# Optimization experiments

Hardware: AMD Instinct MI355X
Metric: run time of the kernel (lower is better)

## Reference

```python
import jax, jax.numpy as jnp
import numpy as np

B, T, E, A = 4, 4096, 512, 64

def setup_inputs() -> dict:
    key = jax.random.key(0)
    k1, k2, k3, k4 = jax.random.split(key, 4)
    embedded = jax.random.normal(k1, (B, T, E), dtype=jnp.float32)
    # torch Linear(E, A, bias=False): weight [A, E], y = x @ W.T. Store as [E, A].
    s = 1.0 / np.sqrt(E)
    Wq = jax.random.uniform(k2, (E, A), dtype=jnp.float32, minval=-s, maxval=s)
    Wk = jax.random.uniform(k3, (E, A), dtype=jnp.float32, minval=-s, maxval=s)
    Wv = jax.random.uniform(k4, (E, A), dtype=jnp.float32, minval=-s, maxval=s)
    return {"embedded": embedded, "Wq": Wq, "Wk": Wk, "Wv": Wv}

def reference(embedded, Wq, Wk, Wv):
    Q = embedded @ Wq  # [B, T, A]
    K = embedded @ Wk
    V = embedded @ Wv
    A_dim = V.shape[-1]
    scores = jnp.einsum('btd,bsd->bts', Q, K) / jnp.sqrt(jnp.float32(A_dim))  # [B, T, T]
    Tlen = scores.shape[-1]
    causal = jnp.tril(jnp.ones((Tlen, Tlen), dtype=bool))
    scores = jnp.where(causal, scores, -jnp.inf)
    attn = jax.nn.softmax(scores, axis=-1)
    out = jnp.einsum('bts,bsd->btd', attn, V)  # [B, T, A]
    return jnp.round(out, 4)
```

## Files before the change

kernel.cpp:

```cpp
#include <hip/hip_runtime.h>

#define B_ 4
#define T_ 4096
#define E_ 512
#define A_ 64
#define SQSCALE 0.1803368801111204f

typedef __attribute__((ext_vector_type(8)))  short bf16x8;
typedef __attribute__((ext_vector_type(8)))  unsigned short ushort8;
typedef __attribute__((ext_vector_type(4)))  unsigned int   u32x4;
typedef __attribute__((ext_vector_type(4)))  float f32x4;
typedef __attribute__((ext_vector_type(16))) float f32x16;

__device__ __forceinline__ unsigned short f2bf(float x) {
    union { float f; unsigned int u; } v; v.f = x;
    unsigned int r = v.u + 0x7fffu + ((v.u >> 16) & 1u);
    return (unsigned short)(r >> 16);
}
__device__ __forceinline__ unsigned cvtpk(float a, float b) {
    unsigned r;
    asm("v_cvt_pk_bf16_f32 %0, %1, %2" : "=v"(r) : "v"(a), "v"(b));
    return r;
}
__device__ __forceinline__ void pls(unsigned &a, unsigned &b) {
    asm("v_permlane32_swap_b32 %0, %1" : "+v"(a), "+v"(b));
}

__global__ __launch_bounds__(256) void prep_w(
    const float* __restrict__ Wq, const float* __restrict__ Wk,
    const float* __restrict__ Wv, unsigned short* __restrict__ Wp)
{
    const int e = blockIdx.x * 256 + threadIdx.x;
    const int nt = e >> 10;
    const int ks = (e >> 6) & 15;
    const int l  = e & 63;
    const int col = nt * 16 + (l & 15);
    const int kb  = ks * 32 + (l >> 4) * 8;
    const float* W = (col < 64) ? Wq : ((col < 128) ? Wk : Wv);
    const int cc = col & 63;
    const float sc = (col < 64) ? SQSCALE : 1.f;
    union { unsigned short s[8]; ushort8 v; } u;
    #pragma unroll
    for (int j = 0; j < 8; ++j) u.s[j] = f2bf(W[(kb + j) * 64 + cc] * sc);
    *(ushort8*)&Wp[(size_t)e * 8] = u.v;
}

__global__ __launch_bounds__(512, 4) void qkv_proj_kernel(
    const float* __restrict__ emb, const unsigned short* __restrict__ Wp,
    unsigned short* __restrict__ Qo, unsigned short* __restrict__ Kp,
    unsigned short* __restrict__ Vp)
{
    __shared__ unsigned short at[32][536];
    __shared__ unsigned short kt[32][72];
    __shared__ unsigned short vt[64][40];
    const int tid = threadIdx.x;
    const long row0 = (long)blockIdx.x * 32;

    {
        const int r = tid >> 4, c16 = tid & 15;
        const float* __restrict__ src = emb + (row0 + r) * 512;
        #pragma unroll
        for (int j = 0; j < 4; ++j) {
            const int col = j * 128 + c16 * 8;
            const float4 x0 = *(const float4*)(src + col);
            const float4 x1 = *(const float4*)(src + col + 4);
            u32x4 p;
            p[0] = cvtpk(x0.x, x0.y); p[1] = cvtpk(x0.z, x0.w);
            p[2] = cvtpk(x1.x, x1.y); p[3] = cvtpk(x1.z, x1.w);
            *(u32x4*)&at[r][col] = p;
        }
    }
    __syncthreads();

    const int w = tid >> 6, lane = tid & 63;
    const int c = lane & 15, hi = lane >> 4;
    const int rg = w & 1, ng = w >> 1;

    f32x4 acc[3];
    #pragma unroll
    for (int j = 0; j < 3; ++j) acc[j] = (f32x4){0.f, 0.f, 0.f, 0.f};

    #pragma unroll
    for (int ks = 0; ks < 16; ++ks) {
        const bf16x8 af = *(const bf16x8*)&at[rg * 16 + c][ks * 32 + hi * 8];
        #pragma unroll
        for (int j = 0; j < 3; ++j) {
            const int nt = ng * 3 + j;
            const bf16x8 bf_ = *(const bf16x8*)&Wp[((size_t)(nt * 16 + ks) * 64 + lane) * 8];
            acc[j] = __builtin_amdgcn_mfma_f32_16x16x32_bf16(af, bf_, acc[j], 0, 0, 0);
        }
    }

    #pragma unroll
    for (int j = 0; j < 3; ++j) {
        const int nt = ng * 3 + j;
        #pragma unroll
        for (int r4 = 0; r4 < 4; ++r4) {
            const int rloc = rg * 16 + hi * 4 + r4;
            const unsigned short v = f2bf(acc[j][r4]);
            if (nt < 4)       Qo[(row0 + rloc) * 64 + nt * 16 + c] = v;
            else if (nt < 8)  kt[rloc][(nt - 4) * 16 + c] = v;
            else              vt[(nt - 8) * 16 + c][rloc] = v;
        }
    }
    __syncthreads();

    const int tloc = (int)(row0 & 4095);
    const long bb = row0 >> 12;
    const int ci  = tloc >> 6;
    const int f_  = (tloc >> 5) & 1;
    const int ks0 = (tloc >> 4) & 3;
    if (tid < 256) {
        const int kk = tid >> 6, l = tid & 63;
        const ushort8 val = *(const ushort8*)&kt[l & 31][kk * 16 + (l >> 5) * 8];
        *(ushort8*)&Kp[((((bb * 64 + ci) * 2 + f_) * 4 + kk) * 64 + l) * 8] = val;
    } else {
        const int e = tid - 256;
        const int ksl = e >> 7, ct = (e >> 6) & 1, l = e & 63;
        const ushort8 val = *(const ushort8*)&vt[ct * 32 + (l & 31)][ksl * 16 + (l >> 5) * 8];
        *(ushort8*)&Vp[((((bb * 64 + ci) * 4 + ks0 + ksl) * 2 + ct) * 64 + l) * 8] = val;
    }
}

__global__ __launch_bounds__(512, 2) void attn_kernel(
    const unsigned short* __restrict__ Q, const unsigned short* __restrict__ Kp,
    const unsigned short* __restrict__ Vp, float* __restrict__ out)
{
    __shared__ float accbuf[8][64][34];
    __shared__ float mbuf[8][32], lbuf[8][32];
    __shared__ float scb[8][32];

    const int tid = threadIdx.x, w = tid >> 6, lane = tid & 63;
    const int c = lane & 31, h = lane >> 5;
    const int b = blockIdx.x & 3;
    const int u = blockIdx.x >> 2;
    const int t = (u < 64) ? (127 - u) : (u - 64);
    const int qb = t << 5;

    const unsigned short* __restrict__ Qb  = Q  + ((long)b * T_ + qb) * 64;
    const unsigned short* __restrict__ Kpb = Kp + (size_t)b * 64 * 8 * 512;
    const unsigned short* __restrict__ Vpb = Vp + (size_t)b * 64 * 8 * 512;

    bf16x8 qf[4];
    #pragma unroll
    for (int kk = 0; kk < 4; ++kk)
        qf[kk] = *(const bf16x8*)&Qb[(long)c * 64 + kk * 16 + h * 8];

    f32x16 acc[2];
    #pragma unroll
    for (int ct = 0; ct < 2; ++ct)
        #pragma unroll
        for (int j = 0; j < 16; ++j) acc[ct][j] = 0.f;
    float m = -1e30f, l = 0.f;

    const int nc = ((qb + 31) >> 6) + 1;

    bf16x8 kf[2][4];
    {
        const size_t cp = (w < nc) ? w : (nc - 1);
        #pragma unroll
        for (int f = 0; f < 2; ++f)
            #pragma unroll
            for (int kk = 0; kk < 4; ++kk)
                kf[f][kk] = *(const bf16x8*)&Kpb[(((cp * 2 + f) * 4 + kk) * 64 + lane) * 8];
    }

    #pragma unroll 2
    for (int ci = w; ci < nc; ci += 8) {
        const long s0 = (long)ci << 6;

        bf16x8 vf[4][2];
        #pragma unroll
        for (int ks = 0; ks < 4; ++ks)
            #pragma unroll
            for (int ct = 0; ct < 2; ++ct)
                vf[ks][ct] = *(const bf16x8*)&Vpb[((((size_t)ci * 4 + ks) * 2 + ct) * 64 + lane) * 8];

        f32x16 sf[2];
        #pragma unroll
        for (int f = 0; f < 2; ++f)
            #pragma unroll
            for (int j = 0; j < 16; ++j) sf[f][j] = 0.f;
        __builtin_amdgcn_s_setprio(1);
        #pragma unroll
        for (int f = 0; f < 2; ++f)
            #pragma unroll
            for (int kk = 0; kk < 4; ++kk)
                sf[f] = __builtin_amdgcn_mfma_f32_32x32x16_bf16(kf[f][kk], qf[kk], sf[f], 0, 0, 0);
        __builtin_amdgcn_s_setprio(0);

        bf16x8 kn[2][4];
        {
            const int cin = ci + 8;
            const size_t cp = (cin < nc) ? cin : (nc - 1);
            #pragma unroll
            for (int f = 0; f < 2; ++f)
                #pragma unroll
                for (int kk = 0; kk < 4; ++kk)
                    kn[f][kk] = *(const bf16x8*)&Kpb[(((cp * 2 + f) * 4 + kk) * 64 + lane) * 8];
        }

        if ((int)s0 + 63 > qb) {
            #pragma unroll
            for (int f = 0; f < 2; ++f)
                #pragma unroll
                for (int r = 0; r < 16; ++r) {
                    const int key = (int)s0 + f * 32 + ((r & 3) + 8 * (r >> 2)) + 4 * h;
                    if (key > qb + c) sf[f][r] = -1e30f;
                }
        }

        float t0 = fmaxf(sf[0][0], sf[1][0]);
        float t1 = fmaxf(sf[0][1], sf[1][1]);
        float t2 = fmaxf(sf[0][2], sf[1][2]);
        float t3 = fmaxf(sf[0][3], sf[1][3]);
        #pragma unroll
        for (int r = 4; r < 16; r += 4) {
            t0 = fmaxf(t0, fmaxf(sf[0][r],     sf[1][r]));
            t1 = fmaxf(t1, fmaxf(sf[0][r + 1], sf[1][r + 1]));
            t2 = fmaxf(t2, fmaxf(sf[0][r + 2], sf[1][r + 2]));
            t3 = fmaxf(t3, fmaxf(sf[0][r + 3], sf[1][r + 3]));
        }
        float pm = fmaxf(fmaxf(t0, t1), fmaxf(t2, t3));
        pm = fmaxf(pm, __shfl_xor(pm, 32));

        float mn = m;
        if (__any(pm > m)) {
            mn = fmaxf(m, pm);
            const float sc = exp2f(m - mn);
            m = mn;
            l *= sc;
            if (h == 0) scb[w][c] = sc;
            asm volatile("s_waitcnt lgkmcnt(0)" ::: "memory");
            __builtin_amdgcn_sched_barrier(0);
            float scr[16];
            #pragma unroll
            for (int r = 0; r < 16; ++r)
                scr[r] = scb[w][((r & 3) + 8 * (r >> 2)) + 4 * h];
            #pragma unroll
            for (int ct = 0; ct < 2; ++ct)
                #pragma unroll
                for (int r = 0; r < 16; ++r) acc[ct][r] *= scr[r];
        }

        float s0a = 0.f, s1a = 0.f, s2a = 0.f, s3a = 0.f;
        #pragma unroll
        for (int f = 0; f < 2; ++f)
            #pragma unroll
            for (int r = 0; r < 16; r += 4) {
                float p0 = exp2f(sf[f][r] - mn);
                float p1 = exp2f(sf[f][r + 1] - mn);
                float p2 = exp2f(sf[f][r + 2] - mn);
                float p3 = exp2f(sf[f][r + 3] - mn);
                sf[f][r] = p0; sf[f][r + 1] = p1; sf[f][r + 2] = p2; sf[f][r + 3] = p3;
                s0a += p0; s1a += p1; s2a += p2; s3a += p3;
            }
        float rs = (s0a + s1a) + (s2a + s3a);
        rs += __shfl_xor(rs, 32);
        l += rs;

        #pragma unroll
        for (int f = 0; f < 2; ++f) {
            unsigned w01 = cvtpk(sf[f][0], sf[f][1]);
            unsigned w23 = cvtpk(sf[f][2], sf[f][3]);
            unsigned w45 = cvtpk(sf[f][4], sf[f][5]);
            unsigned w67 = cvtpk(sf[f][6], sf[f][7]);
            pls(w01, w45); pls(w23, w67);
            union { unsigned uu[4]; bf16x8 v; } pa0, pa1;
            pa0.uu[0] = w01; pa0.uu[1] = w23; pa0.uu[2] = w45; pa0.uu[3] = w67;
            unsigned x01 = cvtpk(sf[f][8],  sf[f][9]);
            unsigned x23 = cvtpk(sf[f][10], sf[f][11]);
            unsigned x45 = cvtpk(sf[f][12], sf[f][13]);
            unsigned x67 = cvtpk(sf[f][14], sf[f][15]);
            pls(x01, x45); pls(x23, x67);
            pa1.uu[0] = x01; pa1.uu[1] = x23; pa1.uu[2] = x45; pa1.uu[3] = x67;
            __builtin_amdgcn_s_setprio(1);
            #pragma unroll
            for (int ct = 0; ct < 2; ++ct) {
                acc[ct] = __builtin_amdgcn_mfma_f32_32x32x16_bf16(pa0.v, vf[2 * f][ct],     acc[ct], 0, 0, 0);
                acc[ct] = __builtin_amdgcn_mfma_f32_32x32x16_bf16(pa1.v, vf[2 * f + 1][ct], acc[ct], 0, 0, 0);
            }
            __builtin_amdgcn_s_setprio(0);
        }

        #pragma unroll
        for (int f = 0; f < 2; ++f)
            #pragma unroll
            for (int kk = 0; kk < 4; ++kk) kf[f][kk] = kn[f][kk];
    }

    if (h == 0) { mbuf[w][c] = m; lbuf[w][c] = l; }
    #pragma unroll
    for (int ct = 0; ct < 2; ++ct)
        #pragma unroll
        for (int g = 0; g < 4; ++g) {
            *(float2*)&accbuf[w][ct * 32 + c][g * 8 + 4 * h] =
                make_float2(acc[ct][4 * g], acc[ct][4 * g + 1]);
            *(float2*)&accbuf[w][ct * 32 + c][g * 8 + 4 * h + 2] =
                make_float2(acc[ct][4 * g + 2], acc[ct][4 * g + 3]);
        }
    __syncthreads();
    #pragma unroll
    for (int i = 0; i < 4; ++i) {
        const int e = tid + i * 512;
        const int q = e >> 6, d = e & 63;
        float ms = mbuf[0][q];
        #pragma unroll
        for (int wv = 1; wv < 8; ++wv) ms = fmaxf(ms, mbuf[wv][q]);
        float ls = 0.f, os = 0.f;
        #pragma unroll
        for (int wv = 0; wv < 8; ++wv) {
            const float e_ = exp2f(mbuf[wv][q] - ms);
            ls += lbuf[wv][q] * e_;
            os += accbuf[wv][d][q] * e_;
        }
        out[((long)b * T_ + qb + q) * 64 + d] = os / ls;
    }
}

extern "C" void kernel_launch(void* const* d_in, const int* in_sizes, int n_in,
                              void* d_out, int out_size, void* d_ws, size_t ws_size,
                              hipStream_t stream)
{
    const float* emb = (const float*)d_in[0];
    const float* Wq  = (const float*)d_in[1];
    const float* Wk  = (const float*)d_in[2];
    const float* Wv  = (const float*)d_in[3];
    float* out = (float*)d_out;

    unsigned short* Qs = (unsigned short*)d_ws;
    unsigned short* Kp = Qs + (size_t)B_ * T_ * A_;
    unsigned short* Vp = Kp + (size_t)B_ * T_ * A_;
    unsigned short* Wp = Vp + (size_t)B_ * T_ * A_;

    prep_w<<<dim3(48), dim3(256), 0, stream>>>(Wq, Wk, Wv, Wp);
    qkv_proj_kernel<<<dim3(512), dim3(512), 0, stream>>>(emb, Wp, Qs, Kp, Vp);
    attn_kernel<<<dim3(512), dim3(512), 0, stream>>>(Qs, Kp, Vp, out);
}
```

Baseline: 53.79 us.

## Swap PV MFMA operands so rescale is per-lane; pack Q in MFMA layout

Swaps the A/B operands of the P·V MFMA so the output accumulator is transposed. Each lane then owns a single query row, which lets the online-softmax rescale use a per-lane scalar instead of broadcasting factors through LDS with a waitcnt. Q is also written in a pre-packed fragment layout from the projection kernel, and the epilogue accbuf layout becomes [q][d] with float4 stores. The unroll-2 pragma on the main loop is removed. The risk is that the layouts of the swapped MFMA fragments do not match, and that dropping the unroll changes scheduling.

```diff
diff --git a/kernel.cpp b/kernel.cpp
--- a/kernel.cpp
+++ b/kernel.cpp
@@ -47,10 +47,11 @@
 
 __global__ __launch_bounds__(512, 4) void qkv_proj_kernel(
     const float* __restrict__ emb, const unsigned short* __restrict__ Wp,
-    unsigned short* __restrict__ Qo, unsigned short* __restrict__ Kp,
+    unsigned short* __restrict__ Qp, unsigned short* __restrict__ Kp,
     unsigned short* __restrict__ Vp)
 {
     __shared__ unsigned short at[32][536];
+    __shared__ unsigned short qt[32][72];
     __shared__ unsigned short kt[32][72];
     __shared__ unsigned short vt[64][40];
     const int tid = threadIdx.x;
@@ -98,7 +99,7 @@
         for (int r4 = 0; r4 < 4; ++r4) {
             const int rloc = rg * 16 + hi * 4 + r4;
             const unsigned short v = f2bf(acc[j][r4]);
-            if (nt < 4)       Qo[(row0 + rloc) * 64 + nt * 16 + c] = v;
+            if (nt < 4)       qt[rloc][nt * 16 + c] = v;
             else if (nt < 8)  kt[rloc][(nt - 4) * 16 + c] = v;
             else              vt[(nt - 8) * 16 + c][rloc] = v;
         }
@@ -110,10 +111,13 @@
     const int ci  = tloc >> 6;
     const int f_  = (tloc >> 5) & 1;
     const int ks0 = (tloc >> 4) & 3;
+    const int tt  = tloc >> 5;
     if (tid < 256) {
         const int kk = tid >> 6, l = tid & 63;
-        const ushort8 val = *(const ushort8*)&kt[l & 31][kk * 16 + (l >> 5) * 8];
-        *(ushort8*)&Kp[((((bb * 64 + ci) * 2 + f_) * 4 + kk) * 64 + l) * 8] = val;
+        const ushort8 kval = *(const ushort8*)&kt[l & 31][kk * 16 + (l >> 5) * 8];
+        *(ushort8*)&Kp[((((bb * 64 + ci) * 2 + f_) * 4 + kk) * 64 + l) * 8] = kval;
+        const ushort8 qval = *(const ushort8*)&qt[l & 31][kk * 16 + (l >> 5) * 8];
+        *(ushort8*)&Qp[(((bb * 128 + tt) * 4 + kk) * 64 + l) * 8] = qval;
     } else {
         const int e = tid - 256;
         const int ksl = e >> 7, ct = (e >> 6) & 1, l = e & 63;
@@ -123,12 +127,11 @@
 }
 
 __global__ __launch_bounds__(512, 2) void attn_kernel(
-    const unsigned short* __restrict__ Q, const unsigned short* __restrict__ Kp,
+    const unsigned short* __restrict__ Qp, const unsigned short* __restrict__ Kp,
     const unsigned short* __restrict__ Vp, float* __restrict__ out)
 {
-    __shared__ float accbuf[8][64][34];
+    __shared__ float accbuf[8][32][68];
     __shared__ float mbuf[8][32], lbuf[8][32];
-    __shared__ float scb[8][32];
 
     const int tid = threadIdx.x, w = tid >> 6, lane = tid & 63;
     const int c = lane & 31, h = lane >> 5;
@@ -137,14 +140,14 @@
     const int t = (u < 64) ? (127 - u) : (u - 64);
     const int qb = t << 5;
 
-    const unsigned short* __restrict__ Qb  = Q  + ((long)b * T_ + qb) * 64;
+    const unsigned short* __restrict__ Qpb = Qp + (size_t)b * 128 * 4 * 512;
     const unsigned short* __restrict__ Kpb = Kp + (size_t)b * 64 * 8 * 512;
     const unsigned short* __restrict__ Vpb = Vp + (size_t)b * 64 * 8 * 512;
 
     bf16x8 qf[4];
     #pragma unroll
     for (int kk = 0; kk < 4; ++kk)
-        qf[kk] = *(const bf16x8*)&Qb[(long)c * 64 + kk * 16 + h * 8];
+        qf[kk] = *(const bf16x8*)&Qpb[(((size_t)t * 4 + kk) * 64 + lane) * 8];
 
     f32x16 acc[2];
     #pragma unroll
@@ -165,7 +168,6 @@
                 kf[f][kk] = *(const bf16x8*)&Kpb[(((cp * 2 + f) * 4 + kk) * 64 + lane) * 8];
     }
 
-    #pragma unroll 2
     for (int ci = w; ci < nc; ci += 8) {
         const long s0 = (long)ci << 6;
 
@@ -230,17 +232,10 @@
             const float sc = exp2f(m - mn);
             m = mn;
             l *= sc;
-            if (h == 0) scb[w][c] = sc;
-            asm volatile("s_waitcnt lgkmcnt(0)" ::: "memory");
-            __builtin_amdgcn_sched_barrier(0);
-            float scr[16];
-            #pragma unroll
-            for (int r = 0; r < 16; ++r)
-                scr[r] = scb[w][((r & 3) + 8 * (r >> 2)) + 4 * h];
             #pragma unroll
             for (int ct = 0; ct < 2; ++ct)
                 #pragma unroll
-                for (int r = 0; r < 16; ++r) acc[ct][r] *= scr[r];
+                for (int r = 0; r < 16; ++r) acc[ct][r] *= sc;
         }
 
         float s0a = 0.f, s1a = 0.f, s2a = 0.f, s3a = 0.f;
@@ -277,8 +272,8 @@
             __builtin_amdgcn_s_setprio(1);
             #pragma unroll
             for (int ct = 0; ct < 2; ++ct) {
-                acc[ct] = __builtin_amdgcn_mfma_f32_32x32x16_bf16(pa0.v, vf[2 * f][ct],     acc[ct], 0, 0, 0);
-                acc[ct] = __builtin_amdgcn_mfma_f32_32x32x16_bf16(pa1.v, vf[2 * f + 1][ct], acc[ct], 0, 0, 0);
+                acc[ct] = __builtin_amdgcn_mfma_f32_32x32x16_bf16(vf[2 * f][ct],     pa0.v, acc[ct], 0, 0, 0);
+                acc[ct] = __builtin_amdgcn_mfma_f32_32x32x16_bf16(vf[2 * f + 1][ct], pa1.v, acc[ct], 0, 0, 0);
             }
             __builtin_amdgcn_s_setprio(0);
         }
@@ -293,12 +288,10 @@
     #pragma unroll
     for (int ct = 0; ct < 2; ++ct)
         #pragma unroll
-        for (int g = 0; g < 4; ++g) {
-            *(float2*)&accbuf[w][ct * 32 + c][g * 8 + 4 * h] =
-                make_float2(acc[ct][4 * g], acc[ct][4 * g + 1]);
-            *(float2*)&accbuf[w][ct * 32 + c][g * 8 + 4 * h + 2] =
-                make_float2(acc[ct][4 * g + 2], acc[ct][4 * g + 3]);
-        }
+        for (int g = 0; g < 4; ++g)
+            *(float4*)&accbuf[w][c][ct * 32 + g * 8 + 4 * h] =
+                make_float4(acc[ct][4 * g], acc[ct][4 * g + 1],
+                            acc[ct][4 * g + 2], acc[ct][4 * g + 3]);
     __syncthreads();
     #pragma unroll
     for (int i = 0; i < 4; ++i) {
@@ -312,7 +305,7 @@
         for (int wv = 0; wv < 8; ++wv) {
             const float e_ = exp2f(mbuf[wv][q] - ms);
             ls += lbuf[wv][q] * e_;
-            os += accbuf[wv][d][q] * e_;
+            os += accbuf[wv][q][d] * e_;
         }
         out[((long)b * T_ + qb + q) * 64 + d] = os / ls;
     }
@@ -328,12 +321,12 @@
     const float* Wv  = (const float*)d_in[3];
     float* out = (float*)d_out;
 
-    unsigned short* Qs = (unsigned short*)d_ws;
-    unsigned short* Kp = Qs + (size_t)B_ * T_ * A_;
+    unsigned short* Qp = (unsigned short*)d_ws;
+    unsigned short* Kp = Qp + (size_t)B_ * T_ * A_;
     unsigned short* Vp = Kp + (size_t)B_ * T_ * A_;
     unsigned short* Wp = Vp + (size_t)B_ * T_ * A_;
 
     prep_w<<<dim3(48), dim3(256), 0, stream>>>(Wq, Wk, Wv, Wp);
-    qkv_proj_kernel<<<dim3(512), dim3(512), 0, stream>>>(emb, Wp, Qs, Kp, Vp);
-    attn_kernel<<<dim3(512), dim3(512), 0, stream>>>(Qs, Kp, Vp, out);
-}
+    qkv_proj_kernel<<<dim3(512), dim3(512), 0, stream>>>(emb, Wp, Qp, Kp, Vp);
+    attn_kernel<<<dim3(512), dim3(512), 0, stream>>>(Qp, Kp, Vp, out);
+}
```

Result: faster. 52.04 us (-3.3%).
